# Performance work log

Measured on AMD Instinct MI355X. Metric: run time of the kernel, lower is better.

The kernel has to match this reference:

```python
import jax, jax.numpy as jnp
import numpy as np

D_MODEL = 1024
N_HEADS = 16
D_K = D_MODEL // N_HEADS  # 64
D_FF = int(8 * D_MODEL / 3)  # 2730
THETA = 10000.0
MAX_SEQ_LEN = 2048
BATCH = 2
SEQ = 2048
EPS = 1e-5


def setup_inputs() -> dict:
    key = jax.random.key(0)
    ks = jax.random.split(key, 10)

    def lin(k, d_out, d_in):
        sigma = np.sqrt(2.0 / (d_out + d_in))
        w = jax.random.truncated_normal(k, -3.0, 3.0, (d_out, d_in), dtype=jnp.float32)
        return w * sigma

    x = jax.random.normal(ks[0], (BATCH, SEQ, D_MODEL), dtype=jnp.float32)
    token_positions = jnp.tile(jnp.arange(SEQ, dtype=jnp.int32)[None, :], (BATCH, 1))
    return {
        "x": x,
        "token_positions": token_positions,
        "WQ": lin(ks[1], D_MODEL, D_MODEL),
        "WK": lin(ks[2], D_MODEL, D_MODEL),
        "WV": lin(ks[3], D_MODEL, D_MODEL),
        "WO": lin(ks[4], D_MODEL, D_MODEL),
        "W1": lin(ks[5], D_FF, D_MODEL),
        "W2": lin(ks[6], D_MODEL, D_FF),
        "W3": lin(ks[7], D_FF, D_MODEL),
        "g1": jnp.ones((D_MODEL,), dtype=jnp.float32),
        "g2": jnp.ones((D_MODEL,), dtype=jnp.float32),
    }


def _rmsnorm(x, g):
    xf = x.astype(jnp.float32)
    inv = jax.lax.rsqrt(jnp.mean(xf * xf, axis=-1, keepdims=True) + EPS)
    return (xf * inv * g).astype(x.dtype)


def _rope(x, pos):
    # x: [b, h, t, d_k]; pos: [b, t] int. Pairs are consecutive (x0,x1).
    half = D_K // 2
    inv_freq = THETA ** (-(2.0 * jnp.arange(1, half + 1, dtype=jnp.float32) - 2.0) / D_K)
    ang = pos.astype(jnp.float32)[..., None] * inv_freq  # [b, t, half]
    cos = jnp.cos(ang)[:, None, :, :]  # [b, 1, t, half]
    sin = jnp.sin(ang)[:, None, :, :]
    xr = x.reshape(*x.shape[:-1], half, 2)
    x0, x1 = xr[..., 0], xr[..., 1]
    out = jnp.stack([cos * x0 - sin * x1, sin * x0 + cos * x1], axis=-1)
    return out.reshape(x.shape)


def reference(x, token_positions, WQ, WK, WV, WO, W1, W2, W3, g1, g2):
    b, t, _ = x.shape
    # --- attention sublayer (pre-norm) ---
    h = _rmsnorm(x, g1)
    q = jnp.einsum('btd,ed->bte', h, WQ).reshape(b, t, N_HEADS, D_K).transpose(0, 2, 1, 3)
    k = jnp.einsum('btd,ed->bte', h, WK).reshape(b, t, N_HEADS, D_K).transpose(0, 2, 1, 3)
    v = jnp.einsum('btd,ed->bte', h, WV).reshape(b, t, N_HEADS, D_K).transpose(0, 2, 1, 3)
    q = _rope(q, token_positions)
    k = _rope(k, token_positions)
    scores = jnp.einsum('bhqd,bhkd->bhqk', q, k) * (D_K ** -0.5)
    causal = jnp.tril(jnp.ones((t, t), dtype=bool))
    scores = jnp.where(causal, scores, -jnp.inf)
    attn = jax.nn.softmax(scores, axis=-1)
    o = jnp.einsum('bhqk,bhkd->bhqd', attn, v)
    o = o.transpose(0, 2, 1, 3).reshape(b, t, D_MODEL)
    o = jnp.einsum('btd,ed->bte', o, WO)
    x = x + o
    # --- SwiGLU FFN sublayer (pre-norm) ---
    h = _rmsnorm(x, g2)
    u = jnp.einsum('btd,fd->btf', h, W1)
    g = jnp.einsum('btd,fd->btf', h, W3)
    ff = jnp.einsum('btf,df->btd', (u * jax.nn.sigmoid(u)) * g, W2)
    return x + ff
```

## Files before the change

kernel.cpp:

```cpp
#include <hip/hip_runtime.h>
#include <cstdint>

#define BT_ROWS 4096
#define DM      1024
#define DFF     2730
#define DFFP    2816
#define TSEQ    2048

typedef float  f32x4  __attribute__((ext_vector_type(4)));
typedef __bf16 bf16x8 __attribute__((ext_vector_type(8)));

typedef __attribute__((address_space(1))) const unsigned int as1_uint;
typedef __attribute__((address_space(3))) unsigned int       as3_uint;

__device__ __forceinline__ unsigned short f2bf(float f) {
  union { float f; unsigned int u; } v; v.f = f;
  unsigned int u = v.u;
  return (unsigned short)((u + 0x7fffu + ((u >> 16) & 1u)) >> 16);
}
__device__ __forceinline__ float bf2f(unsigned int b) {
  union { unsigned int u; float f; } v; v.u = b << 16;
  return v.f;
}

__device__ __forceinline__ void async_cp16(const void* g, void* l) {
  __builtin_amdgcn_global_load_lds((as1_uint*)(uintptr_t)g, (as3_uint*)(uintptr_t)l, 16, 0, 0);
}

#define PREP_GROUPS (1048576L + 1441792L + 720896L + 32768L)
__global__ void prep_kernel(const float* __restrict__ WQ, const float* __restrict__ WK,
                            const float* __restrict__ WV, const float* __restrict__ WOp,
                            const float* __restrict__ W1, const float* __restrict__ W3,
                            const float* __restrict__ W2, const int* __restrict__ pos,
                            unsigned short* __restrict__ Wqkv, unsigned short* __restrict__ Wo,
                            unsigned short* __restrict__ W13i, unsigned short* __restrict__ W2p,
                            float2* __restrict__ cs) {
  long grp = (long)blockIdx.x * 256 + threadIdx.x;
  if (grp < 1048576) {
    const int j = (int)(grp >> 18);
    const long t = (grp & 262143L) * 4;
    const float* s = (j == 0) ? WQ : (j == 1) ? WK : (j == 2) ? WV : WOp;
    unsigned short* d = (j < 3) ? (Wqkv + (size_t)j * 1048576) : Wo;
    const float4 v = *reinterpret_cast<const float4*>(s + t);
    *reinterpret_cast<ushort4*>(d + t) =
        make_ushort4(f2bf(v.x), f2bf(v.y), f2bf(v.z), f2bf(v.w));
    return;
  }
  grp -= 1048576;
  if (grp < 1441792) {
    const int half = (int)(grp / 720896);
    const long t = (grp % 720896) * 4;
    const int r = (int)(t >> 10), c = (int)(t & 1023);
    ushort4 o = make_ushort4(0, 0, 0, 0);
    if (r < DFF) {
      const float4 v = *reinterpret_cast<const float4*>(((half ? W3 : W1) + (long)r * 1024 + c));
      o = make_ushort4(f2bf(v.x), f2bf(v.y), f2bf(v.z), f2bf(v.w));
    }
    *reinterpret_cast<ushort4*>(W13i + ((long)2 * r + half) * 1024 + c) = o;
    return;
  }
  grp -= 1441792;
  if (grp < 720896) {
    const long t = grp * 4;
    const int r = (int)(t / DFFP), c = (int)(t % DFFP);
    const float* src = W2 + (long)r * DFF + c;
    ushort4 o;
    o.x = (c     < DFF) ? f2bf(src[0]) : 0;
    o.y = (c + 1 < DFF) ? f2bf(src[1]) : 0;
    o.z = (c + 2 < DFF) ? f2bf(src[2]) : 0;
    o.w = (c + 3 < DFF) ? f2bf(src[3]) : 0;
    *reinterpret_cast<ushort4*>(W2p + t) = o;
    return;
  }
  grp -= 720896;
  if (grp < 32768) {
    const long i0 = grp * 4;
    const int r = (int)(i0 >> 5);
    const float p = (float)pos[r];
#pragma unroll
    for (int j = 0; j < 4; ++j) {
      const int i = (int)((i0 + j) & 31);
      const float f = powf(10000.f, -(float)(2 * i) * (1.f / 64.f));
      float sv, cv;
      sincosf(p * f, &sv, &cv);
      cs[i0 + j] = make_float2(cv, sv);
    }
  }
}

__global__ void rmsnorm_kernel(const float* __restrict__ x, const float* __restrict__ g,
                               unsigned short* __restrict__ out) {
  const int row = blockIdx.x, tid = threadIdx.x;
  const float4 xv = reinterpret_cast<const float4*>(x + (long)row * DM)[tid];
  float ss = xv.x * xv.x + xv.y * xv.y + xv.z * xv.z + xv.w * xv.w;
#pragma unroll
  for (int o = 32; o > 0; o >>= 1) ss += __shfl_xor(ss, o);
  __shared__ float wsum[4];
  if ((tid & 63) == 0) wsum[tid >> 6] = ss;
  __syncthreads();
  const float inv = rsqrtf((wsum[0] + wsum[1] + wsum[2] + wsum[3]) * (1.f / DM) + 1e-5f);
  const float4 gv = reinterpret_cast<const float4*>(g)[tid];
  ushort4 o4;
  o4.x = f2bf(xv.x * inv * gv.x);
  o4.y = f2bf(xv.y * inv * gv.y);
  o4.z = f2bf(xv.z * inv * gv.z);
  o4.w = f2bf(xv.w * inv * gv.w);
  reinterpret_cast<ushort4*>(out + (long)row * DM)[tid] = o4;
}

__global__ void rmsnorm_bf16_kernel(const unsigned short* __restrict__ x, const float* __restrict__ g,
                                    unsigned short* __restrict__ out) {
  const int row = blockIdx.x, tid = threadIdx.x;
  const ushort4 xu = reinterpret_cast<const ushort4*>(x + (long)row * DM)[tid];
  const float x0 = bf2f(xu.x), x1 = bf2f(xu.y), x2 = bf2f(xu.z), x3 = bf2f(xu.w);
  float ss = x0 * x0 + x1 * x1 + x2 * x2 + x3 * x3;
#pragma unroll
  for (int o = 32; o > 0; o >>= 1) ss += __shfl_xor(ss, o);
  __shared__ float wsum[4];
  if ((tid & 63) == 0) wsum[tid >> 6] = ss;
  __syncthreads();
  const float inv = rsqrtf((wsum[0] + wsum[1] + wsum[2] + wsum[3]) * (1.f / DM) + 1e-5f);
  const float4 gv = reinterpret_cast<const float4*>(g)[tid];
  ushort4 o4;
  o4.x = f2bf(x0 * inv * gv.x);
  o4.y = f2bf(x1 * inv * gv.y);
  o4.z = f2bf(x2 * inv * gv.z);
  o4.w = f2bf(x3 * inv * gv.w);
  reinterpret_cast<ushort4*>(out + (long)row * DM)[tid] = o4;
}

template <int EPI, int BN>
__global__ __launch_bounds__(256) void gemm_bt(
    const unsigned short* __restrict__ A, const unsigned short* __restrict__ B,
    void* __restrict__ C, const float* __restrict__ resid,
    const float2* __restrict__ CS,
    int M, int N, int K, int ldc) {
  constexpr int WNF = BN / 32;
  __shared__ unsigned short As[2][128 * 64];
  __shared__ unsigned short Bs[2][BN * 64];
  const int tid = threadIdx.x;
  const int wid = tid >> 6;
  const int lane = tid & 63;
  const long rowBase = (long)blockIdx.y * 128;
  const long colBase = (long)blockIdx.x * BN;
  const int wm = (wid >> 1) * 64;
  const int wn = (wid & 1) * (BN / 2);
  const int srow = wid * 8 + (lane >> 3);
  const int sc   = lane & 7;
  const int cs   = (sc ^ (srow & 7)) * 8;
  const int fr = lane & 15;
  const int fg = lane >> 4;

  const f32x4 z4 = {0.f, 0.f, 0.f, 0.f};
  f32x4 acc[4][WNF];
#pragma unroll
  for (int m = 0; m < 4; ++m)
#pragma unroll
    for (int n = 0; n < WNF; ++n) acc[m][n] = z4;

  auto stage = [&](int buf, int kt) {
    const long kOff = (long)kt * 64 + cs;
    char* AsB = (char*)As[buf];
    char* BsB = (char*)Bs[buf];
#pragma unroll
    for (int i = 0; i < 4; ++i)
      async_cp16(A + (rowBase + i * 32 + srow) * K + kOff, AsB + i * 4096 + wid * 1024);
#pragma unroll
    for (int i = 0; i < WNF; ++i)
      async_cp16(B + (colBase + i * 32 + srow) * K + kOff, BsB + i * 4096 + wid * 1024);
  };

  const int nkt = K >> 6;
  stage(0, 0);
  __syncthreads();
  for (int kt = 0; kt < nkt; ++kt) {
    if (kt + 1 < nkt) stage((kt + 1) & 1, kt + 1);
    const char* AsB = (const char*)As[kt & 1];
    const char* BsB = (const char*)Bs[kt & 1];
#pragma unroll
    for (int kk = 0; kk < 2; ++kk) {
      bf16x8 af[4], bfr[WNF];
#pragma unroll
      for (int m = 0; m < 4; ++m)
        af[m] = *(const bf16x8*)(AsB + (wm + m * 16 + fr) * 128 + (((kk * 4 + fg) ^ (fr & 7)) * 16));
#pragma unroll
      for (int n = 0; n < WNF; ++n)
        bfr[n] = *(const bf16x8*)(BsB + (wn + n * 16 + fr) * 128 + (((kk * 4 + fg) ^ (fr & 7)) * 16));
#pragma unroll
      for (int m = 0; m < 4; ++m)
#pragma unroll
        for (int n = 0; n < WNF; ++n)
          acc[m][n] = __builtin_amdgcn_mfma_f32_16x16x32_bf16(af[m], bfr[n], acc[m][n], 0, 0, 0);
    }
    __syncthreads();
  }

  const int erow = fg * 4;
  if (EPI == 0) {
    unsigned short* Cp = (unsigned short*)C;
#pragma unroll
    for (int m = 0; m < 4; ++m) {
      const long r0 = rowBase + wm + m * 16 + erow;
#pragma unroll
      for (int n = 0; n < WNF; ++n) {
        const long col = colBase + wn + n * 16 + fr;
#pragma unroll
        for (int r = 0; r < 4; ++r) Cp[(r0 + r) * ldc + col] = f2bf(acc[m][n][r]);
      }
    }
  } else if (EPI == 5) {
    unsigned short* Cp = (unsigned short*)C;
#pragma unroll
    for (int m = 0; m < 4; ++m) {
      const long r0 = rowBase + wm + m * 16 + erow;
#pragma unroll
      for (int n = 0; n < WNF; ++n) {
        const long col = colBase + wn + n * 16 + fr;
#pragma unroll
        for (int r = 0; r < 4; ++r) {
          const long o = (r0 + r) * ldc + col;
          Cp[o] = f2bf(acc[m][n][r] + resid[o]);
        }
      }
    }
  } else if (EPI == 6) {
    float* Cf = (float*)C;
    const unsigned short* Rb = (const unsigned short*)(const void*)resid;
#pragma unroll
    for (int m = 0; m < 4; ++m) {
      const long r0 = rowBase + wm + m * 16 + erow;
#pragma unroll
      for (int n = 0; n < WNF; ++n) {
        const long col = colBase + wn + n * 16 + fr;
#pragma unroll
        for (int r = 0; r < 4; ++r) {
          const long o = (r0 + r) * ldc + col;
          Cf[o] = acc[m][n][r] + bf2f(Rb[o]);
        }
      }
    }
  } else if (EPI == 3) {
    unsigned short* Cp = (unsigned short*)C;
    const int even = !(fr & 1);
#pragma unroll
    for (int m = 0; m < 4; ++m) {
      const long r0 = rowBase + wm + m * 16 + erow;
#pragma unroll
      for (int n = 0; n < WNF; ++n) {
        const long col = colBase + wn + n * 16 + fr;
        const long fcol = col >> 1;
#pragma unroll
        for (int r = 0; r < 4; ++r) {
          const float own = acc[m][n][r];
          const float oth = __shfl_xor(own, 1);
          if (even) {
            const float s = own * oth / (1.f + __expf(-own));
            Cp[(r0 + r) * ldc + fcol] = f2bf(s);
          }
        }
      }
    }
  } else {
    unsigned short* Cp = (unsigned short*)C;
    const int even = !(fr & 1);
#pragma unroll
    for (int m = 0; m < 4; ++m) {
      const long r0 = rowBase + wm + m * 16 + erow;
#pragma unroll
      for (int n = 0; n < WNF; ++n) {
        const long col = colBase + wn + n * 16 + fr;
        const int i = (int)((col & 63) >> 1);
#pragma unroll
        for (int r = 0; r < 4; ++r) {
          const float own = acc[m][n][r];
          const float oth = __shfl_xor(own, 1);
          const float2 cv = CS[(r0 + r) * 32 + i];
          const float v = even ? (cv.x * own - cv.y * oth) : (cv.y * oth + cv.x * own);
          Cp[(r0 + r) * ldc + col] = f2bf(v);
        }
      }
    }
  }
}

#define KSTR 72
__global__ __launch_bounds__(256) void attn_kernel(
    const unsigned short* __restrict__ QK, const unsigned short* __restrict__ Vt,
    unsigned short* __restrict__ O) {
  __shared__ unsigned short Ks[2][64 * KSTR];
  const int bh = blockIdx.x;
  const int b = bh >> 4, h = bh & 15;
  const int tid = threadIdx.x;
  const int wid = tid >> 6, lane = tid & 63;
  const int fr = lane & 15, g = lane >> 4;
  const long rowb = (long)b * TSEQ;
  const int hoff = h * 64;
  const float C2 = 0.18033688011112042f;

  const int ki = tid >> 3;
  const int kcol = (tid & 7) * 8;
  const int kgrow = 8 * ((ki & 15) >> 2) + (ki & 3) + ((ki >> 4) << 2);

  const unsigned short* Kg = QK + rowb * 2048 + 1024 + hoff;
  const unsigned short* Vrow = Vt + (long)(hoff + fr) * 4096 + rowb + g * 8;
  const f32x4 z4 = {0.f, 0.f, 0.f, 0.f};
  bf16x8 onesv;
#pragma unroll
  for (int j = 0; j < 8; ++j) onesv[j] = (__bf16)1.0f;

#pragma unroll
  for (int phase = 0; phase < 2; ++phase) {
    const int qblk = phase ? (31 - blockIdx.y) : blockIdx.y;
    const int qbase = qblk * 64 + wid * 16;
    const int qg = qbase + fr;
    const int nkt = qblk + 1;

    const unsigned short* qrow = QK + (rowb + qbase + fr) * 2048 + hoff + g * 8;
    const bf16x8 qb0 = *reinterpret_cast<const bf16x8*>(qrow);
    const bf16x8 qb1 = *reinterpret_cast<const bf16x8*>(qrow + 32);

    f32x4 acc[4];
#pragma unroll
    for (int d = 0; d < 4; ++d) acc[d] = z4;
    f32x4 accL = z4;
    float mrun = -1e30f;

    uint4 kr0 = *reinterpret_cast<const uint4*>(Kg + (long)kgrow * 2048 + kcol);
    uint4 kr1 = *reinterpret_cast<const uint4*>(Kg + (long)(32 + kgrow) * 2048 + kcol);

    __syncthreads();

    for (int kt = 0; kt < nkt; ++kt) {
      unsigned short* Kb = Ks[kt & 1];
      *reinterpret_cast<uint4*>(&Kb[ki * KSTR + kcol]) = kr0;
      *reinterpret_cast<uint4*>(&Kb[(32 + ki) * KSTR + kcol]) = kr1;
      __syncthreads();
      const int kbase = kt * 64;
      if (kt + 1 < nkt) {
        kr0 = *reinterpret_cast<const uint4*>(Kg + (long)(kbase + 64 + kgrow) * 2048 + kcol);
        kr1 = *reinterpret_cast<const uint4*>(Kg + (long)(kbase + 96 + kgrow) * 2048 + kcol);
      }
      bf16x8 vf[4][2];
#pragma unroll
      for (int db = 0; db < 4; ++db)
#pragma unroll
        for (int ks = 0; ks < 2; ++ks)
          vf[db][ks] = *reinterpret_cast<const bf16x8*>(Vrow + (size_t)db * 16 * 4096 + kbase + ks * 32);

      f32x4 s1[2], s2[2];
#pragma unroll
      for (int ks = 0; ks < 2; ++ks) {
        const unsigned short* ra = &Kb[(ks * 32 + fr) * KSTR];
        const unsigned short* rc = &Kb[(ks * 32 + 16 + fr) * KSTR];
        f32x4 t1 = z4, t2 = z4;
        t1 = __builtin_amdgcn_mfma_f32_16x16x32_bf16(*reinterpret_cast<const bf16x8*>(ra + g * 8), qb0, t1, 0, 0, 0);
        t1 = __builtin_amdgcn_mfma_f32_16x16x32_bf16(*reinterpret_cast<const bf16x8*>(ra + 32 + g * 8), qb1, t1, 0, 0, 0);
        t2 = __builtin_amdgcn_mfma_f32_16x16x32_bf16(*reinterpret_cast<const bf16x8*>(rc + g * 8), qb0, t2, 0, 0, 0);
        t2 = __builtin_amdgcn_mfma_f32_16x16x32_bf16(*reinterpret_cast<const bf16x8*>(rc + 32 + g * 8), qb1, t2, 0, 0, 0);
        s1[ks] = t1; s2[ks] = t2;
      }

      float sc[16];
      if (kt + 1 < nkt) {
#pragma unroll
        for (int ks = 0; ks < 2; ++ks)
#pragma unroll
          for (int j = 0; j < 4; ++j) {
            sc[ks * 8 + j] = s1[ks][j];
            sc[ks * 8 + 4 + j] = s2[ks][j];
          }
      } else {
        const int kb8 = kbase + 8 * g;
#pragma unroll
        for (int ks = 0; ks < 2; ++ks)
#pragma unroll
          for (int j = 0; j < 4; ++j) {
            sc[ks * 8 + j]     = (kb8 + ks * 32 + j     <= qg) ? s1[ks][j] : -1e30f;
            sc[ks * 8 + 4 + j] = (kb8 + ks * 32 + 4 + j <= qg) ? s2[ks][j] : -1e30f;
          }
      }
      const float t0 = fmaxf(fmaxf(sc[0], sc[1]), sc[2]);
      const float t1 = fmaxf(fmaxf(sc[3], sc[4]), sc[5]);
      const float t2 = fmaxf(fmaxf(sc[6], sc[7]), sc[8]);
      const float t3 = fmaxf(fmaxf(sc[9], sc[10]), sc[11]);
      const float t4 = fmaxf(fmaxf(sc[12], sc[13]), sc[14]);
      float tmax = fmaxf(fmaxf(fmaxf(t0, t1), t2), fmaxf(fmaxf(t3, t4), sc[15]));
      const float p1 = __shfl_xor(tmax, 16);
      const float p2 = __shfl_xor(tmax, 32);
      const float p3 = __shfl_xor(tmax, 48);
      tmax = fmaxf(fmaxf(tmax, p1), fmaxf(p2, p3));
      if (__any(tmax > mrun)) {
        const float mnew = fmaxf(mrun, tmax);
        const float alpha = exp2f((mrun - mnew) * C2);
#pragma unroll
        for (int db = 0; db < 4; ++db)
#pragma unroll
          for (int r = 0; r < 4; ++r) acc[db][r] *= alpha;
#pragma unroll
        for (int r = 0; r < 4; ++r) accL[r] *= alpha;
        mrun = mnew;
      }
      const float m2 = mrun * C2;
      bf16x8 pbv[2];
#pragma unroll
      for (int ks = 0; ks < 2; ++ks)
#pragma unroll
        for (int j = 0; j < 8; ++j)
          pbv[ks][j] = (__bf16)exp2f(fmaf(sc[ks * 8 + j], C2, -m2));

#pragma unroll
      for (int db = 0; db < 4; ++db) {
        acc[db] = __builtin_amdgcn_mfma_f32_16x16x32_bf16(vf[db][0], pbv[0], acc[db], 0, 0, 0);
        acc[db] = __builtin_amdgcn_mfma_f32_16x16x32_bf16(vf[db][1], pbv[1], acc[db], 0, 0, 0);
      }
      accL = __builtin_amdgcn_mfma_f32_16x16x32_bf16(onesv, pbv[0], accL, 0, 0, 0);
      accL = __builtin_amdgcn_mfma_f32_16x16x32_bf16(onesv, pbv[1], accL, 0, 0, 0);
    }

    const float inv = 1.f / accL[0];
    unsigned short* orow = O + (rowb + qbase + fr) * DM + hoff;
#pragma unroll
    for (int db = 0; db < 4; ++db) {
      uint2 pk;
      pk.x = (unsigned int)f2bf(acc[db][0] * inv) | ((unsigned int)f2bf(acc[db][1] * inv) << 16);
      pk.y = (unsigned int)f2bf(acc[db][2] * inv) | ((unsigned int)f2bf(acc[db][3] * inv) << 16);
      *reinterpret_cast<uint2*>(orow + db * 16 + g * 4) = pk;
    }
  }
}

static constexpr size_t OFF_WQKV = 0;
static constexpr size_t OFF_WO   = 6291456;
static constexpr size_t OFF_W13  = 8388608;
static constexpr size_t OFF_W2   = 19922944;
static constexpr size_t OFF_H    = 25690112;
static constexpr size_t OFF_X2   = 34078720;
static constexpr size_t OFF_CS   = 50855936;
static constexpr size_t OFF_QK   = 51904512;
static constexpr size_t OFF_VT   = 68681728;
static constexpr size_t OFF_HO   = 77070336;

extern "C" void kernel_launch(void* const* d_in, const int* in_sizes, int n_in,
                              void* d_out, int out_size, void* d_ws, size_t ws_size,
                              hipStream_t stream) {
  const float* x  = (const float*)d_in[0];
  const int* tpos = (const int*)d_in[1];
  const float* WQ = (const float*)d_in[2];
  const float* WK = (const float*)d_in[3];
  const float* WV = (const float*)d_in[4];
  const float* WO = (const float*)d_in[5];
  const float* W1 = (const float*)d_in[6];
  const float* W2 = (const float*)d_in[7];
  const float* W3 = (const float*)d_in[8];
  const float* g1 = (const float*)d_in[9];
  const float* g2 = (const float*)d_in[10];
  float* out = (float*)d_out;

  char* ws = (char*)d_ws;
  unsigned short* Wqkv = (unsigned short*)(ws + OFF_WQKV);
  unsigned short* Wo   = (unsigned short*)(ws + OFF_WO);
  unsigned short* W13i = (unsigned short*)(ws + OFF_W13);
  unsigned short* W2p  = (unsigned short*)(ws + OFF_W2);
  unsigned short* hbuf = (unsigned short*)(ws + OFF_H);
  unsigned short* x2b  = (unsigned short*)(ws + OFF_X2);
  float2* cs           = (float2*)(ws + OFF_CS);
  unsigned short* QKb  = (unsigned short*)(ws + OFF_QK);
  unsigned short* Sbuf = (unsigned short*)(ws + OFF_QK);
  unsigned short* Vtb  = (unsigned short*)(ws + OFF_VT);
  unsigned short* Ho   = (unsigned short*)(ws + OFF_HO);

  prep_kernel<<<(int)(PREP_GROUPS / 256), 256, 0, stream>>>(
      WQ, WK, WV, WO, W1, W3, W2, tpos, Wqkv, Wo, W13i, W2p, cs);

  rmsnorm_kernel<<<BT_ROWS, 256, 0, stream>>>(x, g1, hbuf);
  gemm_bt<4, 128><<<dim3(16, 32), 256, 0, stream>>>(hbuf, Wqkv, QKb, nullptr, cs, BT_ROWS, 2048, 1024, 2048);
  gemm_bt<0, 64><<<dim3(64, 8), 256, 0, stream>>>(Wqkv + 2048 * 1024, hbuf, Vtb, nullptr, nullptr, 1024, BT_ROWS, 1024, BT_ROWS);
  attn_kernel<<<dim3(32, 16), 256, 0, stream>>>(QKb, Vtb, Ho);
  gemm_bt<5, 64><<<dim3(16, 32), 256, 0, stream>>>(Ho, Wo, x2b, x, nullptr, BT_ROWS, 1024, 1024, 1024);

  rmsnorm_bf16_kernel<<<BT_ROWS, 256, 0, stream>>>(x2b, g2, hbuf);
  gemm_bt<3, 128><<<dim3(44, 32), 256, 0, stream>>>(hbuf, W13i, Sbuf, nullptr, nullptr, BT_ROWS, 2 * DFFP, 1024, DFFP);
  gemm_bt<6, 64><<<dim3(16, 32), 256, 0, stream>>>(Sbuf, W2p, out, (const float*)(const void*)x2b, nullptr, BT_ROWS, 1024, DFFP, 1024);
}
```

Baseline: 254.9 us.

## Fuse first RMSNorm into prep kernel and remap GEMM workgroups across XCDs

New measurement: 251.0 us. No clear change (-1.5%).

```diff
diff --git a/kernel.cpp b/kernel.cpp
--- a/kernel.cpp
+++ b/kernel.cpp
@@ -27,14 +27,35 @@
   __builtin_amdgcn_global_load_lds((as1_uint*)(uintptr_t)g, (as3_uint*)(uintptr_t)l, 16, 0, 0);
 }
 
-#define PREP_GROUPS (1048576L + 1441792L + 720896L + 32768L)
+#define PREP_BLOCKS 12672
 __global__ void prep_kernel(const float* __restrict__ WQ, const float* __restrict__ WK,
                             const float* __restrict__ WV, const float* __restrict__ WOp,
                             const float* __restrict__ W1, const float* __restrict__ W3,
                             const float* __restrict__ W2, const int* __restrict__ pos,
                             unsigned short* __restrict__ Wqkv, unsigned short* __restrict__ Wo,
                             unsigned short* __restrict__ W13i, unsigned short* __restrict__ W2p,
-                            float2* __restrict__ cs) {
+                            float2* __restrict__ cs,
+                            const float* __restrict__ x, const float* __restrict__ g1,
+                            unsigned short* __restrict__ hbuf) {
+  if (blockIdx.x >= PREP_BLOCKS) {
+    const int row = blockIdx.x - PREP_BLOCKS, tid = threadIdx.x;
+    const float4 xv = reinterpret_cast<const float4*>(x + (long)row * DM)[tid];
+    float ss = xv.x * xv.x + xv.y * xv.y + xv.z * xv.z + xv.w * xv.w;
+#pragma unroll
+    for (int o = 32; o > 0; o >>= 1) ss += __shfl_xor(ss, o);
+    __shared__ float wsum[4];
+    if ((tid & 63) == 0) wsum[tid >> 6] = ss;
+    __syncthreads();
+    const float inv = rsqrtf((wsum[0] + wsum[1] + wsum[2] + wsum[3]) * (1.f / DM) + 1e-5f);
+    const float4 gv = reinterpret_cast<const float4*>(g1)[tid];
+    ushort4 o4;
+    o4.x = f2bf(xv.x * inv * gv.x);
+    o4.y = f2bf(xv.y * inv * gv.y);
+    o4.z = f2bf(xv.z * inv * gv.z);
+    o4.w = f2bf(xv.w * inv * gv.w);
+    reinterpret_cast<ushort4*>(hbuf + (long)row * DM)[tid] = o4;
+    return;
+  }
   long grp = (long)blockIdx.x * 256 + threadIdx.x;
   if (grp < 1048576) {
     const int j = (int)(grp >> 18);
@@ -88,26 +109,6 @@
   }
 }
 
-__global__ void rmsnorm_kernel(const float* __restrict__ x, const float* __restrict__ g,
-                               unsigned short* __restrict__ out) {
-  const int row = blockIdx.x, tid = threadIdx.x;
-  const float4 xv = reinterpret_cast<const float4*>(x + (long)row * DM)[tid];
-  float ss = xv.x * xv.x + xv.y * xv.y + xv.z * xv.z + xv.w * xv.w;
-#pragma unroll
-  for (int o = 32; o > 0; o >>= 1) ss += __shfl_xor(ss, o);
-  __shared__ float wsum[4];
-  if ((tid & 63) == 0) wsum[tid >> 6] = ss;
-  __syncthreads();
-  const float inv = rsqrtf((wsum[0] + wsum[1] + wsum[2] + wsum[3]) * (1.f / DM) + 1e-5f);
-  const float4 gv = reinterpret_cast<const float4*>(g)[tid];
-  ushort4 o4;
-  o4.x = f2bf(xv.x * inv * gv.x);
-  o4.y = f2bf(xv.y * inv * gv.y);
-  o4.z = f2bf(xv.z * inv * gv.z);
-  o4.w = f2bf(xv.w * inv * gv.w);
-  reinterpret_cast<ushort4*>(out + (long)row * DM)[tid] = o4;
-}
-
 __global__ void rmsnorm_bf16_kernel(const unsigned short* __restrict__ x, const float* __restrict__ g,
                                     unsigned short* __restrict__ out) {
   const int row = blockIdx.x, tid = threadIdx.x;
@@ -141,8 +142,13 @@
   const int tid = threadIdx.x;
   const int wid = tid >> 6;
   const int lane = tid & 63;
-  const long rowBase = (long)blockIdx.y * 128;
-  const long colBase = (long)blockIdx.x * BN;
+  const int nwg = gridDim.x * gridDim.y;
+  int flat = blockIdx.y * gridDim.x + blockIdx.x;
+  flat = (flat & 7) * (nwg >> 3) + (flat >> 3);
+  const int bx = flat % gridDim.x;
+  const int by = flat / gridDim.x;
+  const long rowBase = (long)by * 128;
+  const long colBase = (long)bx * BN;
   const int wm = (wid >> 1) * 64;
   const int wn = (wid & 1) * (BN / 2);
   const int srow = wid * 8 + (lane >> 3);
@@ -469,10 +475,9 @@
   unsigned short* Vtb  = (unsigned short*)(ws + OFF_VT);
   unsigned short* Ho   = (unsigned short*)(ws + OFF_HO);
 
-  prep_kernel<<<(int)(PREP_GROUPS / 256), 256, 0, stream>>>(
-      WQ, WK, WV, WO, W1, W3, W2, tpos, Wqkv, Wo, W13i, W2p, cs);
-
-  rmsnorm_kernel<<<BT_ROWS, 256, 0, stream>>>(x, g1, hbuf);
+  prep_kernel<<<PREP_BLOCKS + BT_ROWS, 256, 0, stream>>>(
+      WQ, WK, WV, WO, W1, W3, W2, tpos, Wqkv, Wo, W13i, W2p, cs, x, g1, hbuf);
+
   gemm_bt<4, 128><<<dim3(16, 32), 256, 0, stream>>>(hbuf, Wqkv, QKb, nullptr, cs, BT_ROWS, 2048, 1024, 2048);
   gemm_bt<0, 64><<<dim3(64, 8), 256, 0, stream>>>(Wqkv + 2048 * 1024, hbuf, Vtb, nullptr, nullptr, 1024, BT_ROWS, 1024, BT_ROWS);
   attn_kernel<<<dim3(32, 16), 256, 0, stream>>>(QKb, Vtb, Ho);
```
